# Kernel tuning notes

Hardware: AMD Instinct MI355X
Metric: run time of the kernel (lower is better)

The kernel has to match this reference:

```python
import jax, jax.numpy as jnp
import numpy as np

HIDDEN = 64
CLUSTERS = 25
NUM_CLASSES = 10
N_NODES = 9600
N_FEAT = 128
B_GRAPHS = 64
NODES_PER_GRAPH = N_NODES // B_GRAPHS


def setup_inputs() -> dict:
    key = jax.random.key(0)
    ks = jax.random.split(key, 16)
    # node features
    x = jax.random.normal(ks[0], (N_NODES, N_FEAT), dtype=jnp.float32)
    # block-diagonal symmetric adjacency (p=0.05 within each graph block)
    seg_ids = jnp.repeat(jnp.arange(B_GRAPHS, dtype=jnp.int32), NODES_PER_GRAPH)
    block_mask = (seg_ids[:, None] == seg_ids[None, :]).astype(jnp.float32)
    r = jax.random.uniform(ks[1], (N_NODES, N_NODES), dtype=jnp.float32)
    a = (r < 0.05).astype(jnp.float32) * block_mask
    a = jnp.maximum(a, a.T)  # symmetrize
    a = a * (1.0 - jnp.eye(N_NODES, dtype=jnp.float32))  # no explicit self loops (GCN adds them)

    def glorot(k, shape):
        lim = np.sqrt(6.0 / (shape[0] + shape[1]))
        return jax.random.uniform(k, shape, dtype=jnp.float32, minval=-lim, maxval=lim)

    params = dict(
        W1=glorot(ks[2], (N_FEAT, HIDDEN)), b1=jnp.zeros((HIDDEN,), jnp.float32),
        W2=glorot(ks[3], (HIDDEN, HIDDEN)), b2=jnp.zeros((HIDDEN,), jnp.float32),
        Wa=glorot(ks[4], (HIDDEN, CLUSTERS)), ba=jnp.zeros((CLUSTERS,), jnp.float32),
        Wp=glorot(ks[5], (HIDDEN, HIDDEN)), bp=jnp.zeros((HIDDEN,), jnp.float32),
        Wc=glorot(ks[6], (HIDDEN, NUM_CLASSES)), bc=jnp.zeros((NUM_CLASSES,), jnp.float32),
    )
    return dict(x=x, a=a, seg_ids=seg_ids, num_graphs=B_GRAPHS, **params)


def _gcn(a, x, W, b):
    n = a.shape[0]
    ah = a + jnp.eye(n, dtype=a.dtype)
    d_isqrt = jax.lax.rsqrt(jnp.maximum(ah.sum(axis=1), 1e-12))
    an = d_isqrt[:, None] * ah * d_isqrt[None, :]
    return an @ (x @ W) + b


def reference(x, a, seg_ids, num_graphs, W1, b1, W2, b2, Wa, ba, Wp, bp, Wc, bc):
    B = int(num_graphs)
    C = CLUSTERS
    N = x.shape[0]
    # --- encode: two GCN layers (dropout = identity at inference) ---
    Z = jax.nn.relu(_gcn(a, x, W1, b1))
    Z = jax.nn.relu(_gcn(a, Z, W2, b2))  # [N, H]
    # --- batched DiffPool ---
    # assignment via GCN, softmax over per-graph clusters
    S = jax.nn.softmax(_gcn(a, Z, Wa, ba), axis=-1)  # [N, C]
    # place each node's assignment row into its graph's cluster block -> block-diagonal S_big [N, B*C]
    cols = seg_ids[:, None].astype(jnp.int32) * C + jnp.arange(C, dtype=jnp.int32)[None, :]
    S_big = jnp.zeros((N, B * C), dtype=S.dtype).at[jnp.arange(N)[:, None], cols].set(S)
    Zp = S_big.T @ Z                 # [B*C, H]
    Ap = S_big.T @ (a @ S_big)       # [B*C, B*C], block diagonal
    # --- post GCN on pooled graph + relu ---
    H = jax.nn.relu(_gcn(Ap, Zp, Wp, bp))  # [B*C, H]
    # --- global sum pool readout over pooled nodes per graph ---
    seg_p = jnp.repeat(jnp.arange(B, dtype=jnp.int32), C)
    G_emb = jax.ops.segment_sum(H, seg_p, num_segments=B)  # [B, H]
    logits = G_emb @ Wc + bc  # [B, num_classes]
    return logits
```

## Files before the change

### kernel.cpp

```cpp
#include <hip/hip_runtime.h>

#define NG   64
#define NPG  150
#define NN   9600
#define NF   128
#define NH   64
#define NC   25
#define NCLS 10
#define ELLW 40

typedef unsigned short u16;
typedef unsigned int   u32;

__global__ void k_prep(const float* __restrict__ a, float* __restrict__ dsi,
                       int* __restrict__ cnt, u16* __restrict__ ell) {
  int g = blockIdx.x, t = threadIdx.x;
  if (t >= NPG) return;
  int n = g * NPG + t;
  const float* arow = a + (size_t)n * NN + (size_t)g * NPG;
  u16* er = ell + (size_t)n * ELLW;
  int deg = 1, c = 1;
  er[0] = (u16)t;
  for (int j = 0; j < NPG; ++j)
    if (arow[j] != 0.f && j != t) { deg++; if (c < ELLW) er[c++] = (u16)j; }
  cnt[n] = c;
  dsi[n] = rsqrtf((float)deg);
}

template <int K>
__global__ void k_mm(const float* __restrict__ A, const float* __restrict__ W,
                     float* __restrict__ C) {
  int idx = blockIdx.x * 256 + threadIdx.x;
  int n = idx >> 6, h = idx & 63;
  const float* ar = A + (size_t)n * K;
  float acc = 0.f;
  for (int k = 0; k < K; ++k) acc = fmaf(ar[k], W[k * NH + h], acc);
  C[(size_t)n * NH + h] = acc;
}

__global__ void k_prop(const float* __restrict__ T, const float* __restrict__ dsi,
                       const int* __restrict__ cnt, const u16* __restrict__ ell,
                       const float* __restrict__ b, float* __restrict__ Z) {
  int idx = blockIdx.x * 256 + threadIdx.x;
  int n = idx >> 6, h = idx & 63;
  int g0 = (n / NPG) * NPG;
  int cn = cnt[n];
  const u16* er = ell + (size_t)n * ELLW;
  float acc = 0.f;
  for (int e = 0; e < cn; ++e) {
    int j = g0 + er[e];
    acc = fmaf(dsi[j], T[(size_t)j * NH + h], acc);
  }
  Z[(size_t)n * NH + h] = fmaxf(fmaf(dsi[n], acc, b[h]), 0.f);
}

__global__ void k_mma(const float* __restrict__ Z2, const float* __restrict__ Wa,
                      float* __restrict__ T3) {
  int idx = blockIdx.x * 256 + threadIdx.x;
  int n = idx >> 5, c = idx & 31;
  if (c >= NC) return;
  const float* zr = Z2 + (size_t)n * NH;
  float acc = 0.f;
  for (int k = 0; k < NH; ++k) acc = fmaf(zr[k], Wa[k * NC + c], acc);
  T3[(size_t)n * 26 + c] = acc;
}

__global__ void k_propa(const float* __restrict__ T3, const float* __restrict__ dsi,
                        const int* __restrict__ cnt, const u16* __restrict__ ell,
                        const float* __restrict__ ba, float* __restrict__ S) {
  int idx = blockIdx.x * 256 + threadIdx.x;
  int n = idx >> 5, c = idx & 31;
  if (c >= NC) return;
  int g0 = (n / NPG) * NPG;
  int cn = cnt[n];
  const u16* er = ell + (size_t)n * ELLW;
  float acc = 0.f;
  for (int e = 0; e < cn; ++e) {
    int j = g0 + er[e];
    acc = fmaf(dsi[j], T3[(size_t)j * 26 + c], acc);
  }
  S[(size_t)n * 26 + c] = fmaf(dsi[n], acc, ba[c]);
}

__global__ void k_soft(float* __restrict__ S) {
  int n = blockIdx.x * 256 + threadIdx.x;
  if (n >= NN) return;
  float* r = S + (size_t)n * 26;
  float mx = r[0];
  for (int c = 1; c < NC; ++c) mx = fmaxf(mx, r[c]);
  float s = 0.f;
  for (int c = 0; c < NC; ++c) { float e = expf(r[c] - mx); r[c] = e; s += e; }
  float inv = 1.f / s;
  for (int c = 0; c < NC; ++c) r[c] *= inv;
}

__global__ void k_as(const float* __restrict__ S, const int* __restrict__ cnt,
                     const u16* __restrict__ ell, float* __restrict__ AS) {
  int idx = blockIdx.x * 256 + threadIdx.x;
  int n = idx >> 5, c = idx & 31;
  if (c >= NC) return;
  int g0 = (n / NPG) * NPG;
  int cn = cnt[n];
  const u16* er = ell + (size_t)n * ELLW;
  float acc = 0.f;
  for (int e = 1; e < cn; ++e) {
    int j = g0 + er[e];
    acc += S[(size_t)j * 26 + c];
  }
  AS[(size_t)n * 26 + c] = acc;
}

__global__ void k_zp(const float* __restrict__ S, const float* __restrict__ Z2,
                     float* __restrict__ Zp) {
  int idx = blockIdx.x * 256 + threadIdx.x;
  int g = idx / 1600, rem = idx % 1600;
  int r = rem >> 6, h = rem & 63;
  float acc = 0.f;
  for (int i = 0; i < NPG; ++i) {
    int n = g * NPG + i;
    acc = fmaf(S[(size_t)n * 26 + r], Z2[(size_t)n * NH + h], acc);
  }
  Zp[(size_t)(g * NC + r) * NH + h] = acc;
}

__global__ void k_ap(const float* __restrict__ S, const float* __restrict__ AS,
                     float* __restrict__ Ap) {
  int idx = blockIdx.x * 256 + threadIdx.x;
  if (idx >= NG * 650) return;
  int g = idx / 650, rem = idx % 650;
  int r = rem / 26, c = rem % 26;
  if (c >= NC) return;
  float acc = 0.f;
  for (int i = 0; i < NPG; ++i) {
    int n = g * NPG + i;
    acc = fmaf(S[(size_t)n * 26 + r], AS[(size_t)n * 26 + c], acc);
  }
  Ap[(size_t)(g * NC + r) * 26 + c] = acc;
}

__global__ void k_dsip(const float* __restrict__ Ap, float* __restrict__ dsiP) {
  int idx = blockIdx.x * 256 + threadIdx.x;
  if (idx >= NG * NC) return;
  const float* r = Ap + (size_t)idx * 26;
  float d = 1.f;
  for (int c = 0; c < NC; ++c) d += r[c];
  dsiP[idx] = rsqrtf(d);
}

__global__ void k_u(const float* __restrict__ Zp, const float* __restrict__ Wp,
                    const float* __restrict__ dsiP, float* __restrict__ U) {
  int idx = blockIdx.x * 256 + threadIdx.x;
  int p = idx >> 6, h = idx & 63;
  const float* zr = Zp + (size_t)p * NH;
  float acc = 0.f;
  for (int k = 0; k < NH; ++k) acc = fmaf(zr[k], Wp[k * NH + h], acc);
  U[(size_t)p * NH + h] = dsiP[p] * acc;
}

__global__ void k_hp(const float* __restrict__ U, const float* __restrict__ Ap,
                     const float* __restrict__ dsiP, const float* __restrict__ bp,
                     float* __restrict__ Hp) {
  int idx = blockIdx.x * 256 + threadIdx.x;
  int p = idx >> 6, h = idx & 63;
  int g = p / NC;
  float acc = U[(size_t)p * NH + h];
  const float* apr = Ap + (size_t)p * 26;
  for (int c = 0; c < NC; ++c)
    acc = fmaf(apr[c], U[(size_t)(g * NC + c) * NH + h], acc);
  Hp[(size_t)p * NH + h] = fmaxf(fmaf(dsiP[p], acc, bp[h]), 0.f);
}

__global__ void k_g(const float* __restrict__ Hp, float* __restrict__ G) {
  int idx = blockIdx.x * 256 + threadIdx.x;
  int g = idx >> 6, h = idx & 63;
  float s = 0.f;
  for (int r = 0; r < NC; ++r) s += Hp[(size_t)(g * NC + r) * NH + h];
  G[idx] = s;
}

__global__ void k_out(const float* __restrict__ G, const float* __restrict__ Wc,
                      const float* __restrict__ bc, float* __restrict__ out) {
  int idx = blockIdx.x * 256 + threadIdx.x;
  if (idx >= NG * NCLS) return;
  int g = idx / NCLS, cl = idx % NCLS;
  float acc = bc[cl];
  const float* gr = G + (size_t)g * NH;
  for (int h = 0; h < NH; ++h) acc = fmaf(gr[h], Wc[h * NCLS + cl], acc);
  out[idx] = acc;
}

extern "C" void kernel_launch(void* const* d_in, const int* in_sizes, int n_in,
                              void* d_out, int out_size, void* d_ws, size_t ws_size,
                              hipStream_t stream) {
  (void)in_sizes; (void)n_in; (void)out_size; (void)ws_size;
  const float* x  = (const float*)d_in[0];
  const float* a  = (const float*)d_in[1];
  const float* W1 = (const float*)d_in[4];
  const float* b1 = (const float*)d_in[5];
  const float* W2 = (const float*)d_in[6];
  const float* b2 = (const float*)d_in[7];
  const float* Wa = (const float*)d_in[8];
  const float* ba = (const float*)d_in[9];
  const float* Wp = (const float*)d_in[10];
  const float* bp = (const float*)d_in[11];
  const float* Wc = (const float*)d_in[12];
  const float* bc = (const float*)d_in[13];
  float* out = (float*)d_out;

  char* ws = (char*)d_ws;
  float* dsi  = (float*)(ws + 0);
  int*   cnt  = (int*)  (ws + 38400);
  u16*   ell  = (u16*)  (ws + 76800);
  float* T1   = (float*)(ws + 844800);
  float* Z1   = (float*)(ws + 3302400);
  float* T2   = (float*)(ws + 5760000);
  float* Z2   = (float*)(ws + 8217600);
  float* T3   = (float*)(ws + 10675200);
  float* S    = (float*)(ws + 11673600);
  float* AS   = (float*)(ws + 12672000);
  float* Zp   = (float*)(ws + 13670400);
  float* Ap   = (float*)(ws + 14080000);
  float* dsiP = (float*)(ws + 14246400);
  float* U    = (float*)(ws + 14252800);
  float* Hp   = (float*)(ws + 14662400);
  float* G    = (float*)(ws + 15072000);

  k_prep <<<NG,   256, 0, stream>>>(a, dsi, cnt, ell);
  k_mm<NF><<<2400, 256, 0, stream>>>(x, W1, T1);
  k_prop <<<2400, 256, 0, stream>>>(T1, dsi, cnt, ell, b1, Z1);
  k_mm<NH><<<2400, 256, 0, stream>>>(Z1, W2, T2);
  k_prop <<<2400, 256, 0, stream>>>(T2, dsi, cnt, ell, b2, Z2);
  k_mma  <<<1200, 256, 0, stream>>>(Z2, Wa, T3);
  k_propa<<<1200, 256, 0, stream>>>(T3, dsi, cnt, ell, ba, S);
  k_soft <<<38,   256, 0, stream>>>(S);
  k_as   <<<1200, 256, 0, stream>>>(S, cnt, ell, AS);
  k_zp   <<<400,  256, 0, stream>>>(S, Z2, Zp);
  k_ap   <<<163,  256, 0, stream>>>(S, AS, Ap);
  k_dsip <<<7,    256, 0, stream>>>(Ap, dsiP);
  k_u    <<<400,  256, 0, stream>>>(Zp, Wp, dsiP, U);
  k_hp   <<<400,  256, 0, stream>>>(U, Ap, dsiP, bp, Hp);
  k_g    <<<16,   256, 0, stream>>>(Hp, G);
  k_out  <<<3,    256, 0, stream>>>(G, Wc, bc, out);
}
```

Before: 592.6 us.

## Fuse whole GCN-DiffPool pipeline into one per-graph kernel

Replaces sixteen separate kernel launches with a single kernel that runs one 512-thread block per graph. Each block keeps its graph's ELL adjacency, degrees, softmax assignments and pooled tensors in shared memory, and uses a per-graph global scratch slice for the hidden activations. This is meant to remove launch overhead and the global round trips between stages. In exchange, only 64 blocks run on the GPU and the x@W1 matmul is done per thread without tiling, so compute parallelism is much lower.

```diff
diff --git a/kernel.cpp b/kernel.cpp
--- a/kernel.cpp
+++ b/kernel.cpp
@@ -10,183 +10,177 @@
 #define ELLW 40
 
 typedef unsigned short u16;
-typedef unsigned int   u32;
-
-__global__ void k_prep(const float* __restrict__ a, float* __restrict__ dsi,
-                       int* __restrict__ cnt, u16* __restrict__ ell) {
-  int g = blockIdx.x, t = threadIdx.x;
-  if (t >= NPG) return;
-  int n = g * NPG + t;
-  const float* arow = a + (size_t)n * NN + (size_t)g * NPG;
-  u16* er = ell + (size_t)n * ELLW;
-  int deg = 1, c = 1;
-  er[0] = (u16)t;
-  for (int j = 0; j < NPG; ++j)
-    if (arow[j] != 0.f && j != t) { deg++; if (c < ELLW) er[c++] = (u16)j; }
-  cnt[n] = c;
-  dsi[n] = rsqrtf((float)deg);
-}
-
-template <int K>
-__global__ void k_mm(const float* __restrict__ A, const float* __restrict__ W,
-                     float* __restrict__ C) {
-  int idx = blockIdx.x * 256 + threadIdx.x;
-  int n = idx >> 6, h = idx & 63;
-  const float* ar = A + (size_t)n * K;
-  float acc = 0.f;
-  for (int k = 0; k < K; ++k) acc = fmaf(ar[k], W[k * NH + h], acc);
-  C[(size_t)n * NH + h] = acc;
-}
-
-__global__ void k_prop(const float* __restrict__ T, const float* __restrict__ dsi,
-                       const int* __restrict__ cnt, const u16* __restrict__ ell,
-                       const float* __restrict__ b, float* __restrict__ Z) {
-  int idx = blockIdx.x * 256 + threadIdx.x;
-  int n = idx >> 6, h = idx & 63;
-  int g0 = (n / NPG) * NPG;
-  int cn = cnt[n];
-  const u16* er = ell + (size_t)n * ELLW;
-  float acc = 0.f;
-  for (int e = 0; e < cn; ++e) {
-    int j = g0 + er[e];
-    acc = fmaf(dsi[j], T[(size_t)j * NH + h], acc);
-  }
-  Z[(size_t)n * NH + h] = fmaxf(fmaf(dsi[n], acc, b[h]), 0.f);
-}
-
-__global__ void k_mma(const float* __restrict__ Z2, const float* __restrict__ Wa,
-                      float* __restrict__ T3) {
-  int idx = blockIdx.x * 256 + threadIdx.x;
-  int n = idx >> 5, c = idx & 31;
-  if (c >= NC) return;
-  const float* zr = Z2 + (size_t)n * NH;
-  float acc = 0.f;
-  for (int k = 0; k < NH; ++k) acc = fmaf(zr[k], Wa[k * NC + c], acc);
-  T3[(size_t)n * 26 + c] = acc;
-}
-
-__global__ void k_propa(const float* __restrict__ T3, const float* __restrict__ dsi,
-                        const int* __restrict__ cnt, const u16* __restrict__ ell,
-                        const float* __restrict__ ba, float* __restrict__ S) {
-  int idx = blockIdx.x * 256 + threadIdx.x;
-  int n = idx >> 5, c = idx & 31;
-  if (c >= NC) return;
-  int g0 = (n / NPG) * NPG;
-  int cn = cnt[n];
-  const u16* er = ell + (size_t)n * ELLW;
-  float acc = 0.f;
-  for (int e = 0; e < cn; ++e) {
-    int j = g0 + er[e];
-    acc = fmaf(dsi[j], T3[(size_t)j * 26 + c], acc);
-  }
-  S[(size_t)n * 26 + c] = fmaf(dsi[n], acc, ba[c]);
-}
-
-__global__ void k_soft(float* __restrict__ S) {
-  int n = blockIdx.x * 256 + threadIdx.x;
-  if (n >= NN) return;
-  float* r = S + (size_t)n * 26;
-  float mx = r[0];
-  for (int c = 1; c < NC; ++c) mx = fmaxf(mx, r[c]);
-  float s = 0.f;
-  for (int c = 0; c < NC; ++c) { float e = expf(r[c] - mx); r[c] = e; s += e; }
-  float inv = 1.f / s;
-  for (int c = 0; c < NC; ++c) r[c] *= inv;
-}
-
-__global__ void k_as(const float* __restrict__ S, const int* __restrict__ cnt,
-                     const u16* __restrict__ ell, float* __restrict__ AS) {
-  int idx = blockIdx.x * 256 + threadIdx.x;
-  int n = idx >> 5, c = idx & 31;
-  if (c >= NC) return;
-  int g0 = (n / NPG) * NPG;
-  int cn = cnt[n];
-  const u16* er = ell + (size_t)n * ELLW;
-  float acc = 0.f;
-  for (int e = 1; e < cn; ++e) {
-    int j = g0 + er[e];
-    acc += S[(size_t)j * 26 + c];
-  }
-  AS[(size_t)n * 26 + c] = acc;
-}
-
-__global__ void k_zp(const float* __restrict__ S, const float* __restrict__ Z2,
-                     float* __restrict__ Zp) {
-  int idx = blockIdx.x * 256 + threadIdx.x;
-  int g = idx / 1600, rem = idx % 1600;
-  int r = rem >> 6, h = rem & 63;
-  float acc = 0.f;
-  for (int i = 0; i < NPG; ++i) {
-    int n = g * NPG + i;
-    acc = fmaf(S[(size_t)n * 26 + r], Z2[(size_t)n * NH + h], acc);
-  }
-  Zp[(size_t)(g * NC + r) * NH + h] = acc;
-}
-
-__global__ void k_ap(const float* __restrict__ S, const float* __restrict__ AS,
-                     float* __restrict__ Ap) {
-  int idx = blockIdx.x * 256 + threadIdx.x;
-  if (idx >= NG * 650) return;
-  int g = idx / 650, rem = idx % 650;
-  int r = rem / 26, c = rem % 26;
-  if (c >= NC) return;
-  float acc = 0.f;
-  for (int i = 0; i < NPG; ++i) {
-    int n = g * NPG + i;
-    acc = fmaf(S[(size_t)n * 26 + r], AS[(size_t)n * 26 + c], acc);
-  }
-  Ap[(size_t)(g * NC + r) * 26 + c] = acc;
-}
-
-__global__ void k_dsip(const float* __restrict__ Ap, float* __restrict__ dsiP) {
-  int idx = blockIdx.x * 256 + threadIdx.x;
-  if (idx >= NG * NC) return;
-  const float* r = Ap + (size_t)idx * 26;
-  float d = 1.f;
-  for (int c = 0; c < NC; ++c) d += r[c];
-  dsiP[idx] = rsqrtf(d);
-}
-
-__global__ void k_u(const float* __restrict__ Zp, const float* __restrict__ Wp,
-                    const float* __restrict__ dsiP, float* __restrict__ U) {
-  int idx = blockIdx.x * 256 + threadIdx.x;
-  int p = idx >> 6, h = idx & 63;
-  const float* zr = Zp + (size_t)p * NH;
-  float acc = 0.f;
-  for (int k = 0; k < NH; ++k) acc = fmaf(zr[k], Wp[k * NH + h], acc);
-  U[(size_t)p * NH + h] = dsiP[p] * acc;
-}
-
-__global__ void k_hp(const float* __restrict__ U, const float* __restrict__ Ap,
-                     const float* __restrict__ dsiP, const float* __restrict__ bp,
-                     float* __restrict__ Hp) {
-  int idx = blockIdx.x * 256 + threadIdx.x;
-  int p = idx >> 6, h = idx & 63;
-  int g = p / NC;
-  float acc = U[(size_t)p * NH + h];
-  const float* apr = Ap + (size_t)p * 26;
-  for (int c = 0; c < NC; ++c)
-    acc = fmaf(apr[c], U[(size_t)(g * NC + c) * NH + h], acc);
-  Hp[(size_t)p * NH + h] = fmaxf(fmaf(dsiP[p], acc, bp[h]), 0.f);
-}
-
-__global__ void k_g(const float* __restrict__ Hp, float* __restrict__ G) {
-  int idx = blockIdx.x * 256 + threadIdx.x;
-  int g = idx >> 6, h = idx & 63;
-  float s = 0.f;
-  for (int r = 0; r < NC; ++r) s += Hp[(size_t)(g * NC + r) * NH + h];
-  G[idx] = s;
-}
-
-__global__ void k_out(const float* __restrict__ G, const float* __restrict__ Wc,
-                      const float* __restrict__ bc, float* __restrict__ out) {
-  int idx = blockIdx.x * 256 + threadIdx.x;
-  if (idx >= NG * NCLS) return;
-  int g = idx / NCLS, cl = idx % NCLS;
-  float acc = bc[cl];
-  const float* gr = G + (size_t)g * NH;
-  for (int h = 0; h < NH; ++h) acc = fmaf(gr[h], Wc[h * NCLS + cl], acc);
-  out[idx] = acc;
+
+#define GSTRIDE 24576
+
+__global__ __launch_bounds__(512, 1) void k_fused(
+    const float* __restrict__ x, const float* __restrict__ a,
+    const float* __restrict__ W1, const float* __restrict__ b1,
+    const float* __restrict__ W2, const float* __restrict__ b2,
+    const float* __restrict__ Wa, const float* __restrict__ ba,
+    const float* __restrict__ Wp, const float* __restrict__ bp,
+    const float* __restrict__ Wc, const float* __restrict__ bc,
+    float* ws, float* __restrict__ out) {
+  __shared__ u16   ell[NPG * ELLW];
+  __shared__ int   cnt[NPG];
+  __shared__ float dsi[NPG];
+  __shared__ float S[NPG * 26];
+  __shared__ float Zp[NC * NH];
+  __shared__ float Ap[NC * 26];
+  __shared__ float dsiP[NC];
+  __shared__ float U[NC * NH];
+  __shared__ float Hp[NC * NH];
+  __shared__ float G[NH];
+
+  const int g = blockIdx.x, t = threadIdx.x;
+  float* bufA = ws + (size_t)g * GSTRIDE;
+  float* bufB = bufA + 9600;
+  float* bufC = bufA + 19200;
+
+  if (t < NPG) {
+    const float* arow = a + (size_t)(g * NPG + t) * NN + (size_t)g * NPG;
+    u16* er = ell + t * ELLW;
+    int deg = 1, c = 1;
+    er[0] = (u16)t;
+    for (int j = 0; j < NPG; ++j)
+      if (arow[j] != 0.f && j != t) { deg++; if (c < ELLW) er[c++] = (u16)j; }
+    cnt[t] = c;
+    dsi[t] = rsqrtf((float)deg);
+  }
+  __syncthreads();
+
+  for (int idx = t; idx < NPG * NH; idx += 512) {
+    int i = idx >> 6, h = idx & 63;
+    const float* xr = x + (size_t)(g * NPG + i) * NF;
+    float acc = 0.f;
+    for (int k = 0; k < NF; ++k) acc = fmaf(xr[k], W1[k * NH + h], acc);
+    bufA[idx] = acc;
+  }
+  __syncthreads();
+
+  for (int idx = t; idx < NPG * NH; idx += 512) {
+    int i = idx >> 6, h = idx & 63;
+    int cn = cnt[i];
+    const u16* er = ell + i * ELLW;
+    float acc = 0.f;
+    for (int e = 0; e < cn; ++e) { int j = er[e]; acc = fmaf(dsi[j], bufA[j * NH + h], acc); }
+    bufB[idx] = fmaxf(fmaf(dsi[i], acc, b1[h]), 0.f);
+  }
+  __syncthreads();
+
+  for (int idx = t; idx < NPG * NH; idx += 512) {
+    int i = idx >> 6, h = idx & 63;
+    const float* zr = bufB + i * NH;
+    float acc = 0.f;
+    for (int k = 0; k < NH; ++k) acc = fmaf(zr[k], W2[k * NH + h], acc);
+    bufA[idx] = acc;
+  }
+  __syncthreads();
+
+  for (int idx = t; idx < NPG * NH; idx += 512) {
+    int i = idx >> 6, h = idx & 63;
+    int cn = cnt[i];
+    const u16* er = ell + i * ELLW;
+    float acc = 0.f;
+    for (int e = 0; e < cn; ++e) { int j = er[e]; acc = fmaf(dsi[j], bufA[j * NH + h], acc); }
+    bufB[idx] = fmaxf(fmaf(dsi[i], acc, b2[h]), 0.f);
+  }
+  __syncthreads();
+
+  for (int idx = t; idx < NPG * 26; idx += 512) {
+    int i = idx / 26, c = idx - i * 26;
+    if (c < NC) {
+      const float* zr = bufB + i * NH;
+      float acc = 0.f;
+      for (int k = 0; k < NH; ++k) acc = fmaf(zr[k], Wa[k * NC + c], acc);
+      bufC[i * 26 + c] = acc;
+    }
+  }
+  __syncthreads();
+
+  for (int idx = t; idx < NPG * 26; idx += 512) {
+    int i = idx / 26, c = idx - i * 26;
+    if (c < NC) {
+      int cn = cnt[i];
+      const u16* er = ell + i * ELLW;
+      float acc = 0.f;
+      for (int e = 0; e < cn; ++e) { int j = er[e]; acc = fmaf(dsi[j], bufC[j * 26 + c], acc); }
+      S[i * 26 + c] = fmaf(dsi[i], acc, ba[c]);
+    }
+  }
+  __syncthreads();
+  if (t < NPG) {
+    float* r = S + t * 26;
+    float mx = r[0];
+    for (int c = 1; c < NC; ++c) mx = fmaxf(mx, r[c]);
+    float s = 0.f;
+    for (int c = 0; c < NC; ++c) { float e = expf(r[c] - mx); r[c] = e; s += e; }
+    float inv = 1.f / s;
+    for (int c = 0; c < NC; ++c) r[c] *= inv;
+  }
+  __syncthreads();
+
+  for (int idx = t; idx < NPG * 26; idx += 512) {
+    int i = idx / 26, c = idx - i * 26;
+    if (c < NC) {
+      int cn = cnt[i];
+      const u16* er = ell + i * ELLW;
+      float acc = 0.f;
+      for (int e = 1; e < cn; ++e) { int j = er[e]; acc += S[j * 26 + c]; }
+      bufC[i * 26 + c] = acc;
+    }
+  }
+  __syncthreads();
+
+  for (int idx = t; idx < NC * NH; idx += 512) {
+    int r = idx >> 6, h = idx & 63;
+    float acc = 0.f;
+    for (int i = 0; i < NPG; ++i) acc = fmaf(S[i * 26 + r], bufB[i * NH + h], acc);
+    Zp[idx] = acc;
+  }
+  for (int idx = t; idx < NC * NC; idx += 512) {
+    int r = idx / NC, c = idx - r * NC;
+    float acc = 0.f;
+    for (int i = 0; i < NPG; ++i) acc = fmaf(S[i * 26 + r], bufC[i * 26 + c], acc);
+    Ap[r * 26 + c] = acc;
+  }
+  __syncthreads();
+
+  if (t < NC) {
+    float d = 1.f;
+    for (int c = 0; c < NC; ++c) d += Ap[t * 26 + c];
+    dsiP[t] = rsqrtf(d);
+  }
+  __syncthreads();
+
+  for (int idx = t; idx < NC * NH; idx += 512) {
+    int r = idx >> 6, h = idx & 63;
+    float acc = 0.f;
+    for (int k = 0; k < NH; ++k) acc = fmaf(Zp[r * NH + k], Wp[k * NH + h], acc);
+    U[idx] = dsiP[r] * acc;
+  }
+  __syncthreads();
+
+  for (int idx = t; idx < NC * NH; idx += 512) {
+    int r = idx >> 6, h = idx & 63;
+    float acc = U[idx];
+    for (int c = 0; c < NC; ++c) acc = fmaf(Ap[r * 26 + c], U[c * NH + h], acc);
+    Hp[idx] = fmaxf(fmaf(dsiP[r], acc, bp[h]), 0.f);
+  }
+  __syncthreads();
+
+  if (t < NH) {
+    float s = 0.f;
+    for (int r = 0; r < NC; ++r) s += Hp[r * NH + t];
+    G[t] = s;
+  }
+  __syncthreads();
+
+  if (t < NCLS) {
+    float acc = bc[t];
+    for (int h = 0; h < NH; ++h) acc = fmaf(G[h], Wc[h * NCLS + t], acc);
+    out[g * NCLS + t] = acc;
+  }
 }
 
 extern "C" void kernel_launch(void* const* d_in, const int* in_sizes, int n_in,
@@ -205,40 +199,7 @@
   const float* bp = (const float*)d_in[11];
   const float* Wc = (const float*)d_in[12];
   const float* bc = (const float*)d_in[13];
-  float* out = (float*)d_out;
-
-  char* ws = (char*)d_ws;
-  float* dsi  = (float*)(ws + 0);
-  int*   cnt  = (int*)  (ws + 38400);
-  u16*   ell  = (u16*)  (ws + 76800);
-  float* T1   = (float*)(ws + 844800);
-  float* Z1   = (float*)(ws + 3302400);
-  float* T2   = (float*)(ws + 5760000);
-  float* Z2   = (float*)(ws + 8217600);
-  float* T3   = (float*)(ws + 10675200);
-  float* S    = (float*)(ws + 11673600);
-  float* AS   = (float*)(ws + 12672000);
-  float* Zp   = (float*)(ws + 13670400);
-  float* Ap   = (float*)(ws + 14080000);
-  float* dsiP = (float*)(ws + 14246400);
-  float* U    = (float*)(ws + 14252800);
-  float* Hp   = (float*)(ws + 14662400);
-  float* G    = (float*)(ws + 15072000);
-
-  k_prep <<<NG,   256, 0, stream>>>(a, dsi, cnt, ell);
-  k_mm<NF><<<2400, 256, 0, stream>>>(x, W1, T1);
-  k_prop <<<2400, 256, 0, stream>>>(T1, dsi, cnt, ell, b1, Z1);
-  k_mm<NH><<<2400, 256, 0, stream>>>(Z1, W2, T2);
-  k_prop <<<2400, 256, 0, stream>>>(T2, dsi, cnt, ell, b2, Z2);
-  k_mma  <<<1200, 256, 0, stream>>>(Z2, Wa, T3);
-  k_propa<<<1200, 256, 0, stream>>>(T3, dsi, cnt, ell, ba, S);
-  k_soft <<<38,   256, 0, stream>>>(S);
-  k_as   <<<1200, 256, 0, stream>>>(S, cnt, ell, AS);
-  k_zp   <<<400,  256, 0, stream>>>(S, Z2, Zp);
-  k_ap   <<<163,  256, 0, stream>>>(S, AS, Ap);
-  k_dsip <<<7,    256, 0, stream>>>(Ap, dsiP);
-  k_u    <<<400,  256, 0, stream>>>(Zp, Wp, dsiP, U);
-  k_hp   <<<400,  256, 0, stream>>>(U, Ap, dsiP, bp, Hp);
-  k_g    <<<16,   256, 0, stream>>>(Hp, G);
-  k_out  <<<3,    256, 0, stream>>>(G, Wc, bc, out);
+
+  k_fused<<<NG, 512, 0, stream>>>(x, a, W1, b1, W2, b2, Wa, ba, Wp, bp, Wc, bc,
+                                  (float*)d_ws, (float*)d_out);
 }
```

After: 665.9 us. +12.4%, slower.
